# Performance work log

Hardware: AMD Instinct MI355X
Metric: run time of the kernel (lower is better)

The kernel has to match this reference:

```python
import jax, jax.numpy as jnp
import numpy as np

EPS_LN = 1e-6   # ln_1 / ln_2 (partial(LayerNorm, eps=1e-6))
EPS_ON = 1e-5   # SS2D out_norm (default LayerNorm eps)


def _ln(x, g, b, eps):
    m = jnp.mean(x, -1, keepdims=True)
    v = jnp.mean(jnp.square(x - m), -1, keepdims=True)
    return (x - m) * jax.lax.rsqrt(v + eps) * g + b


def _dwconv(x, w, b):
    # x: (B,C,H,W), w: (C,1,3,3) depthwise, 'SAME' padding (padding=1 for k=3)
    y = jax.lax.conv_general_dilated(x, w, (1, 1), 'SAME',
        feature_group_count=x.shape[1], dimension_numbers=('NCHW', 'OIHW', 'NCHW'))
    return y + b[None, :, None, None]


def _selective_scan(u, dts, A, Bs, Cs, Ds):
    # u, dts: (B,K,D,L); A: (K,D,N); Bs, Cs: (B,K,N,L); Ds: (K,D)
    B, K, D, L = u.shape
    N = A.shape[-1]
    uT = jnp.moveaxis(u, -1, 0)    # (L,B,K,D)
    dtT = jnp.moveaxis(dts, -1, 0)  # (L,B,K,D)
    BT = jnp.moveaxis(Bs, -1, 0)   # (L,B,K,N)
    CT = jnp.moveaxis(Cs, -1, 0)   # (L,B,K,N)

    def step(h, inp):
        u_t, dt_t, B_t, C_t = inp
        dA = jnp.exp(dt_t[..., None] * A)                                   # (B,K,D,N)
        h = dA * h + (dt_t * u_t)[..., None] * B_t[:, :, None, :]           # (B,K,D,N)
        y = jnp.einsum('bkdn,bkn->bkd', h, C_t)
        return h, y

    h0 = jnp.zeros((B, K, D, N), u.dtype)
    _, ys = jax.lax.scan(step, h0, (uT, dtT, BT, CT))
    ys = jnp.moveaxis(ys, 0, -1)   # (B,K,D,L)
    return ys + u * Ds[None, :, :, None]


def _ss2d(x, in_proj_w, conv_w, conv_b, x_proj_w, dt_w, dt_b, A_logs, Ds,
          onorm_g, onorm_b, out_proj_w):
    # x: (B,H,W,C) -> (B,H,W,C)
    B, H, W, C = x.shape
    Di = in_proj_w.shape[0] // 2
    K = x_proj_w.shape[0]
    R = dt_w.shape[-1]
    N = (x_proj_w.shape[1] - R) // 2
    L = H * W

    xz = x @ in_proj_w.T                       # (B,H,W,2*Di), bias=False
    xx, z = jnp.split(xz, 2, axis=-1)
    xx = jnp.transpose(xx, (0, 3, 1, 2))       # (B,Di,H,W)
    xx = jax.nn.silu(_dwconv(xx, conv_w, conv_b))

    # cross-scan: row-major, col-major, and their reversals
    x0 = xx.reshape(B, Di, L)
    x1 = jnp.transpose(xx, (0, 1, 3, 2)).reshape(B, Di, L)
    xs = jnp.stack([x0, x1, x0[..., ::-1], x1[..., ::-1]], axis=1)  # (B,K,Di,L)

    x_dbl = jnp.einsum('bkdl,kcd->bkcl', xs, x_proj_w)
    dts, Bs, Cs = jnp.split(x_dbl, [R, R + N], axis=2)
    dts = jnp.einsum('bkrl,kdr->bkdl', dts, dt_w)
    dts = jax.nn.softplus(dts + dt_b[None, :, :, None])
    A = -jnp.exp(A_logs.reshape(K, Di, N))

    ys = _selective_scan(xs, dts, A, Bs, Cs, Ds.reshape(K, Di))  # (B,K,Di,L)

    # cross-merge back to row-major
    y0 = ys[:, 0]
    y1 = jnp.transpose(ys[:, 1].reshape(B, Di, W, H), (0, 1, 3, 2)).reshape(B, Di, L)
    y2 = ys[:, 2, :, ::-1]
    y3 = jnp.transpose(ys[:, 3, :, ::-1].reshape(B, Di, W, H), (0, 1, 3, 2)).reshape(B, Di, L)
    y = jnp.transpose(y0 + y1 + y2 + y3, (0, 2, 1))              # (B,L,Di)
    y = _ln(y, onorm_g, onorm_b, EPS_ON).reshape(B, H, W, Di)
    y = y * jax.nn.silu(z)
    return y @ out_proj_w.T                    # bias=False


def setup_inputs() -> dict:
    key = jax.random.key(0)
    ks = jax.random.split(key, 16)
    B, H, W, C = 2, 56, 56, 192
    Di, N, K = 2 * C, 16, 4
    R = int(np.ceil(C / 16))                   # dt_rank = 12
    hid = 4 * C
    g = lambda k, shp, s=0.02: (jax.random.normal(k, shp) * s).astype(jnp.float32)
    return dict(
        x=jax.random.normal(ks[0], (B, H, W, C), jnp.float32),
        cpe1_w=g(ks[1], (C, 1, 3, 3), 0.1), cpe1_b=jnp.zeros((C,), jnp.float32),
        ln1_g=jnp.ones((C,), jnp.float32), ln1_b=jnp.zeros((C,), jnp.float32),
        in_proj_w=g(ks[2], (2 * Di, C)),
        conv_w=g(ks[3], (Di, 1, 3, 3), 0.1), conv_b=jnp.zeros((Di,), jnp.float32),
        x_proj_w=g(ks[4], (K, R + 2 * N, Di)),
        dt_w=g(ks[5], (K, Di, R), 0.1),
        dt_b=jnp.full((K, Di), float(np.log(np.expm1(0.01))), jnp.float32),
        A_logs=jnp.log(jnp.tile(jnp.arange(1, N + 1, dtype=jnp.float32), (K * Di, 1))),
        Ds=jnp.ones((K * Di,), jnp.float32),
        onorm_g=jnp.ones((Di,), jnp.float32), onorm_b=jnp.zeros((Di,), jnp.float32),
        out_proj_w=g(ks[6], (C, Di)),
        cpe2_w=g(ks[7], (C, 1, 3, 3), 0.1), cpe2_b=jnp.zeros((C,), jnp.float32),
        ln2_g=jnp.ones((C,), jnp.float32), ln2_b=jnp.zeros((C,), jnp.float32),
        fc1_w=g(ks[8], (hid, C)), fc1_b=jnp.zeros((hid,), jnp.float32),
        fc2_w=g(ks[9], (C, hid)), fc2_b=jnp.zeros((C,), jnp.float32),
    )


def reference(x, cpe1_w, cpe1_b, ln1_g, ln1_b, in_proj_w, conv_w, conv_b,
              x_proj_w, dt_w, dt_b, A_logs, Ds, onorm_g, onorm_b, out_proj_w,
              cpe2_w, cpe2_b, ln2_g, ln2_b, fc1_w, fc1_b, fc2_w, fc2_b):
    # x: (B,H,W,C)
    x = x + jnp.transpose(_dwconv(jnp.transpose(x, (0, 3, 1, 2)), cpe1_w, cpe1_b), (0, 2, 3, 1))
    x = x + _ss2d(_ln(x, ln1_g, ln1_b, EPS_LN), in_proj_w, conv_w, conv_b,
                  x_proj_w, dt_w, dt_b, A_logs, Ds, onorm_g, onorm_b, out_proj_w)
    x = x + jnp.transpose(_dwconv(jnp.transpose(x, (0, 3, 1, 2)), cpe2_w, cpe2_b), (0, 2, 3, 1))
    h = _ln(x, ln2_g, ln2_b, EPS_LN)
    h = jax.nn.gelu(h @ fc1_w.T + fc1_b, approximate=False)
    x = x + (h @ fc2_w.T + fc2_b)
    return x
```

## Files before the change

kernel.cpp:

```cpp
#include <hip/hip_runtime.h>
#include <math.h>

#define BB 2
#define HHH 56
#define WWW 56
#define CC 192
#define LL 3136
#define DI 384
#define KK 4
#define NN 16
#define RR 12
#define CP 44
#define HIDN 768
#define BL (BB*LL)
#define NCH 98
#define CHL 32

typedef __attribute__((ext_vector_type(8))) short bf16x8;
typedef __attribute__((ext_vector_type(4))) float f32x4;

__device__ __forceinline__ float siluf_(float x){ return x/(1.f+__expf(-x)); }
__device__ __forceinline__ float geluf_(float x){ return 0.5f*x*(1.f+erff(x*0.70710678118654752f)); }
__device__ __forceinline__ unsigned short bf16r_(float x){
  unsigned int u = __float_as_uint(x);
  u += 0x7FFFu + ((u>>16)&1u);
  return (unsigned short)(u>>16);
}
__device__ __forceinline__ float bf2f_(unsigned short u){
  return __uint_as_float(((unsigned int)u)<<16);
}

__global__ void k_cvtw(const float* __restrict__ s0, const float* __restrict__ s1,
                       const float* __restrict__ s2, const float* __restrict__ s3,
                       unsigned short* __restrict__ dst){
  int i = blockIdx.x*256 + threadIdx.x;
  if      (i < 147456) dst[i] = bf16r_(s0[i]);
  else if (i < 221184) dst[i] = bf16r_(s1[i-147456]);
  else if (i < 368640) dst[i] = bf16r_(s2[i-221184]);
  else if (i < 516096) dst[i] = bf16r_(s3[i-368640]);
}

__global__ void k_prepx(const float* __restrict__ xp, unsigned short* __restrict__ wXhi,
                        unsigned short* __restrict__ wXlo){
  int idx = blockIdx.x*256 + threadIdx.x;
  if (idx >= 192*384) return;
  int row = idx / 384, d = idx % 384;
  int k = row / 48, j = row % 48;
  float v = 0.f;
  if (j < 12) v = xp[(k*CP + j)*DI + d];
  else if (j >= 16) v = xp[(k*CP + (j-4))*DI + d];
  unsigned short hi = bf16r_(v);
  wXhi[idx] = hi;
  wXlo[idx] = bf16r_(v - bf2f_(hi));
}

__global__ void k_dwconv_res(const float* __restrict__ in, const float* __restrict__ wgt,
                             const float* __restrict__ bias, float* __restrict__ out) {
  int idx = blockIdx.x*256 + threadIdx.x;
  const int total = BB*HHH*WWW*CC;
  if (idx >= total) return;
  int c = idx % CC;
  int w = (idx / CC) % WWW;
  int h = (idx / (CC*WWW)) % HHH;
  int b = idx / (CC*WWW*HHH);
  float acc = bias[c];
  #pragma unroll
  for (int kh=0; kh<3; kh++){
    int hh = h + kh - 1; if (hh < 0 || hh >= HHH) continue;
    #pragma unroll
    for (int kw=0; kw<3; kw++){
      int ww = w + kw - 1; if (ww < 0 || ww >= WWW) continue;
      acc += in[((b*HHH+hh)*WWW+ww)*CC + c] * wgt[c*9 + kh*3 + kw];
    }
  }
  out[idx] = in[idx] + acc;
}

__global__ void k_ln192(const float* __restrict__ in, const float* __restrict__ g,
                        const float* __restrict__ bta, unsigned short* __restrict__ out, float eps) {
  int row = blockIdx.x*4 + (threadIdx.x>>6);
  int lane = threadIdx.x & 63;
  const float* p = in + (size_t)row*CC;
  float v0=p[lane], v1=p[lane+64], v2=p[lane+128];
  float s = v0+v1+v2, s2 = v0*v0+v1*v1+v2*v2;
  #pragma unroll
  for (int off=1; off<64; off<<=1){ s += __shfl_xor(s,off); s2 += __shfl_xor(s2,off); }
  float m = s*(1.f/192.f);
  float var = s2*(1.f/192.f) - m*m;
  float rstd = rsqrtf(var + eps);
  unsigned short* q = out + (size_t)row*CC;
  q[lane]     = bf16r_((v0-m)*rstd*g[lane]     + bta[lane]);
  q[lane+64]  = bf16r_((v1-m)*rstd*g[lane+64]  + bta[lane+64]);
  q[lane+128] = bf16r_((v2-m)*rstd*g[lane+128] + bta[lane+128]);
}

enum { EPI_NONE=0, EPI_RES=1, EPI_BIAS_GELU=2, EPI_BIAS_RES=3 };

template<int EPI, int OUTBF>
__global__ __launch_bounds__(256) void k_gemm_mfma(const unsigned short* __restrict__ A,
      const unsigned short* __restrict__ W, const float* __restrict__ bias,
      const float* __restrict__ res, void* __restrict__ outp, int M, int Nn, int Kk) {
  __shared__ unsigned short As[128][40];
  __shared__ unsigned short Bs[64][40];
  int tid = threadIdx.x;
  int m0 = blockIdx.y*128, n0 = blockIdx.x*64;
  int wid = tid>>6, lane = tid&63;
  int wm = wid*32;
  int fr = lane&15, fk = (lane>>4)*8;
  f32x4 acc[2][4];
  #pragma unroll
  for (int i=0;i<2;i++)
    #pragma unroll
    for (int j=0;j<4;j++) acc[i][j] = (f32x4){0.f,0.f,0.f,0.f};
  int arow = tid>>1, ak = (tid&1)*16;
  int wrow = tid>>2, wk = (tid&3)*8;
  const unsigned short* Ap = A + (size_t)(m0+arow)*Kk + ak;
  const unsigned short* Wp = W + (size_t)(n0+wrow)*Kk + wk;
  for (int k0=0; k0<Kk; k0+=32){
    __syncthreads();
    uint4 av0 = *(const uint4*)(Ap + k0);
    uint4 av1 = *(const uint4*)(Ap + k0 + 8);
    uint4 wv  = *(const uint4*)(Wp + k0);
    *(uint4*)&As[arow][ak]   = av0;
    *(uint4*)&As[arow][ak+8] = av1;
    *(uint4*)&Bs[wrow][wk]   = wv;
    __syncthreads();
    bf16x8 af[2], bfr[4];
    #pragma unroll
    for (int mi=0;mi<2;mi++) af[mi] = *(const bf16x8*)&As[wm + mi*16 + fr][fk];
    #pragma unroll
    for (int ni=0;ni<4;ni++) bfr[ni] = *(const bf16x8*)&Bs[ni*16 + fr][fk];
    #pragma unroll
    for (int mi=0;mi<2;mi++)
      #pragma unroll
      for (int ni=0;ni<4;ni++)
        acc[mi][ni] = __builtin_amdgcn_mfma_f32_16x16x32_bf16(af[mi], bfr[ni], acc[mi][ni], 0,0,0);
  }
  int rbase = (lane>>4)*4;
  #pragma unroll
  for (int mi=0;mi<2;mi++){
    #pragma unroll
    for (int ni=0;ni<4;ni++){
      int col = n0 + ni*16 + fr;
      float bv = (EPI==EPI_BIAS_GELU || EPI==EPI_BIAS_RES) ? bias[col] : 0.f;
      #pragma unroll
      for (int r=0;r<4;r++){
        int row = m0 + wm + mi*16 + rbase + r;
        float v = acc[mi][ni][r] + bv;
        if (EPI==EPI_BIAS_GELU) v = geluf_(v);
        if (EPI==EPI_RES || EPI==EPI_BIAS_RES) v += res[(size_t)row*Nn + col];
        if (OUTBF) ((unsigned short*)outp)[(size_t)row*Nn + col] = bf16r_(v);
        else       ((float*)outp)[(size_t)row*Nn + col] = v;
      }
    }
  }
}

__global__ __launch_bounds__(256) void k_xgemm(const float* __restrict__ uf,
      const unsigned short* __restrict__ wXhi, const unsigned short* __restrict__ wXlo,
      float* __restrict__ xdblT) {
  __shared__ unsigned short Ah[64][40];
  __shared__ unsigned short Al[64][40];
  __shared__ unsigned short Bh[64][40];
  __shared__ unsigned short Bl[64][40];
  int tid = threadIdx.x;
  int m0 = blockIdx.y*64, n0 = blockIdx.x*64;
  int wid = tid>>6, lane = tid&63;
  int fr = lane&15, fk = (lane>>4)*8;
  f32x4 acc[4];
  #pragma unroll
  for (int j=0;j<4;j++) acc[j] = (f32x4){0.f,0.f,0.f,0.f};
  int srow = tid>>2, sk = (tid&3)*8;
  const float* Ap = uf + (size_t)(m0+srow)*DI + sk;
  const unsigned short* Wh = wXhi + (size_t)(n0+srow)*DI + sk;
  const unsigned short* Wl = wXlo + (size_t)(n0+srow)*DI + sk;
  for (int k0=0; k0<DI; k0+=32){
    __syncthreads();
    float4 ua = *(const float4*)(Ap + k0);
    float4 ub = *(const float4*)(Ap + k0 + 4);
    uint4 wh = *(const uint4*)(Wh + k0);
    uint4 wl = *(const uint4*)(Wl + k0);
    float uv[8] = {ua.x,ua.y,ua.z,ua.w, ub.x,ub.y,ub.z,ub.w};
    #pragma unroll
    for (int j=0;j<8;j++){
      unsigned short hi = bf16r_(uv[j]);
      Ah[srow][sk+j] = hi;
      Al[srow][sk+j] = bf16r_(uv[j] - bf2f_(hi));
    }
    *(uint4*)&Bh[srow][sk] = wh;
    *(uint4*)&Bl[srow][sk] = wl;
    __syncthreads();
    bf16x8 ah = *(const bf16x8*)&Ah[wid*16 + fr][fk];
    bf16x8 al = *(const bf16x8*)&Al[wid*16 + fr][fk];
    #pragma unroll
    for (int ni=0;ni<4;ni++){
      bf16x8 bh = *(const bf16x8*)&Bh[ni*16 + fr][fk];
      bf16x8 bl = *(const bf16x8*)&Bl[ni*16 + fr][fk];
      acc[ni] = __builtin_amdgcn_mfma_f32_16x16x32_bf16(ah, bh, acc[ni], 0,0,0);
      acc[ni] = __builtin_amdgcn_mfma_f32_16x16x32_bf16(al, bh, acc[ni], 0,0,0);
      acc[ni] = __builtin_amdgcn_mfma_f32_16x16x32_bf16(ah, bl, acc[ni], 0,0,0);
    }
  }
  int rbase = (lane>>4)*4;
  #pragma unroll
  for (int ni=0;ni<4;ni++){
    int col = n0 + ni*16 + fr;
    int k = col / 48, j = col % 48;
    #pragma unroll
    for (int r=0;r<4;r++){
      int row = m0 + wid*16 + rbase + r;
      int b = row / LL, s = row % LL;
      int h = s / WWW, w2 = s % WWW;
      int l1 = w2*HHH + h;
      int lk = (k==0) ? s : (k==1) ? l1 : (k==2) ? (LL-1-s) : (LL-1-l1);
      xdblT[((size_t)((b*KK+k)*LL + lk))*48 + j] = acc[ni][r];
    }
  }
}

__global__ void k_conv_xx(const float* __restrict__ xz, const float* __restrict__ cw,
                          const float* __restrict__ cb, float* __restrict__ xc0,
                          float* __restrict__ xc1) {
  int idx = blockIdx.x*256 + threadIdx.x;
  if (idx >= BB*LL*DI) return;
  int d = idx % DI;
  int l = (idx / DI) % LL;
  int b = idx / (DI*LL);
  int h = l / WWW, w = l % WWW;
  float acc = cb[d];
  #pragma unroll
  for (int kh=0; kh<3; kh++){
    int hh = h + kh - 1; if (hh < 0 || hh >= HHH) continue;
    #pragma unroll
    for (int kw=0; kw<3; kw++){
      int ww2 = w + kw - 1; if (ww2 < 0 || ww2 >= WWW) continue;
      acc += xz[((size_t)(b*LL + hh*WWW + ww2))*(2*DI) + d] * cw[d*9 + kh*3 + kw];
    }
  }
  float v = siluf_(acc);
  xc0[idx] = v;
  xc1[((size_t)(b*LL + w*HHH + h))*DI + d] = v;
}

template<int PASS>
__global__ __launch_bounds__(64) void k_scan(const float* __restrict__ xc_l0,
        const float* __restrict__ xc_l1,
        const float* __restrict__ xdblT, const float* __restrict__ dtw, const float* __restrict__ dtb,
        const float* __restrict__ alogs, const float* __restrict__ Dsv,
        float* __restrict__ hend, float* __restrict__ sumdt, unsigned short* __restrict__ ysb) {
  int ch = blockIdx.y, bk = blockIdx.z;
  int b = bk >> 2, k = bk & 3;
  int d = blockIdx.x*64 + threadIdx.x;
  int kd = k*DI + d;
  float w[12];
  #pragma unroll
  for (int r=0;r<12;r++) w[r] = dtw[kd*12 + r];
  float biasd = dtb[kd];
  float Dd = (PASS==1) ? Dsv[kd] : 0.f;
  float An2[16];
  #pragma unroll
  for (int n=0;n<16;n++) An2[n] = -__expf(alogs[kd*16 + n]) * 1.44269504f;
  bool pw = true;
  #pragma unroll
  for (int n=1;n<16;n++) pw = pw && (fabsf(An2[n] - (float)(n+1)*An2[0]) <= 1e-3f*(float)(n+1)*fabsf(An2[0]));
  const float* usrc = (k & 1) ? xc_l1 : xc_l0;
  bool rev = (k >= 2);
  const float* rec0 = xdblT + ((size_t)bk*LL + ch*CHL)*48;
  float h[16];
  size_t hb = ((size_t)(bk*NCH + ch)*DI + d)*16;
  if (PASS==0){
    #pragma unroll
    for (int n=0;n<16;n++) h[n]=0.f;
  } else {
    #pragma unroll
    for (int n4=0;n4<4;n4++){
      float4 hv = *(const float4*)&hend[hb + n4*4];
      h[n4*4]=hv.x; h[n4*4+1]=hv.y; h[n4*4+2]=hv.z; h[n4*4+3]=hv.w;
    }
  }
  float cum = 0.f;
  #pragma unroll 2
  for (int i=0;i<CHL;i++){
    int li = ch*CHL + i;
    int lsrc = rev ? (LL-1-li) : li;
    float uu = usrc[((size_t)(b*LL + lsrc))*DI + d];
    const float* rec = rec0 + (size_t)i*48;
    float4 t0 = *(const float4*)(rec);
    float4 t1 = *(const float4*)(rec+4);
    float4 t2 = *(const float4*)(rec+8);
    float4 B0 = *(const float4*)(rec+16);
    float4 B1 = *(const float4*)(rec+20);
    float4 B2 = *(const float4*)(rec+24);
    float4 B3 = *(const float4*)(rec+28);
    float a0 = fmaf(t0.x,w[0], fmaf(t0.y,w[1], fmaf(t0.z,w[2], t0.w*w[3])));
    float a1 = fmaf(t1.x,w[4], fmaf(t1.y,w[5], fmaf(t1.z,w[6], t1.w*w[7])));
    float a2 = fmaf(t2.x,w[8], fmaf(t2.y,w[9], fmaf(t2.z,w[10], t2.w*w[11])));
    float a = biasd + a0 + (a1 + a2);
    float dt = 0.69314718f * log2f(1.f + exp2f(a*1.44269504f));
    float dtu = dt*uu;
    if (PASS==0) cum += dt;
    float dA[16];
    if (pw){
      float r = exp2f(dt*An2[0]);
      float p = r; dA[0] = p;
      #pragma unroll
      for (int n=1;n<16;n++){ p *= r; dA[n] = p; }
    } else {
      #pragma unroll
      for (int n=0;n<16;n++) dA[n] = exp2f(dt*An2[n]);
    }
    float Bv[16] = {B0.x,B0.y,B0.z,B0.w, B1.x,B1.y,B1.z,B1.w,
                    B2.x,B2.y,B2.z,B2.w, B3.x,B3.y,B3.z,B3.w};
    #pragma unroll
    for (int n=0;n<16;n++) h[n] = fmaf(dA[n], h[n], dtu*Bv[n]);
    if (PASS==1){
      float4 C0 = *(const float4*)(rec+32);
      float4 C1 = *(const float4*)(rec+36);
      float4 C2 = *(const float4*)(rec+40);
      float4 C3 = *(const float4*)(rec+44);
      float y0 = fmaf(h[0], C0.x, fmaf(h[1], C0.y, fmaf(h[2], C0.z, h[3]*C0.w)));
      float y1 = fmaf(h[4], C1.x, fmaf(h[5], C1.y, fmaf(h[6], C1.z, h[7]*C1.w)));
      float y2 = fmaf(h[8], C2.x, fmaf(h[9], C2.y, fmaf(h[10],C2.z, h[11]*C2.w)));
      float y3 = fmaf(h[12],C3.x, fmaf(h[13],C3.y, fmaf(h[14],C3.z, h[15]*C3.w)));
      float y = fmaf(uu, Dd, (y0+y1)+(y2+y3));
      ysb[((size_t)(bk*LL + li))*DI + d] = bf16r_(y);
    }
  }
  if (PASS==0){
    #pragma unroll
    for (int n4=0;n4<4;n4++)
      *(float4*)&hend[hb + n4*4] = make_float4(h[n4*4],h[n4*4+1],h[n4*4+2],h[n4*4+3]);
    sumdt[(bk*NCH + ch)*DI + d] = cum;
  }
}

__global__ __launch_bounds__(64) void k_scanmid(const float* __restrict__ alogs,
        const float* __restrict__ sumdt, float* __restrict__ hend) {
  int bid = blockIdx.x;
  int dblk = bid % 96;
  int k = (bid/96) % KK;
  int b = bid/(96*KK);
  int lane = threadIdx.x;
  int d4 = lane>>4, n = lane&15;
  int d = dblk*4 + d4;
  int bk = b*KK + k;
  float Ac2 = -__expf(alogs[(k*DI+d)*16 + n]) * 1.44269504f;
  float H = 0.f;
  for (int c=0;c<NCH;c++){
    float sdt = sumdt[(bk*NCH + c)*DI + d];
    float aexp = exp2f(Ac2 * sdt);
    size_t idx = ((size_t)(bk*NCH + c)*DI + dblk*4)*16 + lane;
    float tmp = hend[idx];
    hend[idx] = H;
    H = fmaf(aexp, H, tmp);
  }
}

__global__ __launch_bounds__(384) void k_fuse(const unsigned short* __restrict__ ysb,
      const float* __restrict__ xz, const float* __restrict__ og, const float* __restrict__ ob,
      unsigned short* __restrict__ a2) {
  __shared__ float sa[6], sb[6];
  int b = blockIdx.x / LL, l = blockIdx.x % LL;
  int d = threadIdx.x;
  int h_ = l / WWW, w_ = l % WWW;
  int l1 = w_*HHH + h_;
  float y = bf2f_(ysb[((size_t)((b*KK+0)*LL + l))*DI + d])
          + bf2f_(ysb[((size_t)((b*KK+1)*LL + l1))*DI + d])
          + bf2f_(ysb[((size_t)((b*KK+2)*LL + (LL-1-l)))*DI + d])
          + bf2f_(ysb[((size_t)((b*KK+3)*LL + (LL-1-l1)))*DI + d]);
  float s = y, s2 = y*y;
  #pragma unroll
  for (int off=1; off<64; off<<=1){ s += __shfl_xor(s,off); s2 += __shfl_xor(s2,off); }
  int wid = d >> 6;
  if ((d & 63) == 0){ sa[wid] = s; sb[wid] = s2; }
  __syncthreads();
  s = sa[0]+sa[1]+sa[2]+sa[3]+sa[4]+sa[5];
  s2 = sb[0]+sb[1]+sb[2]+sb[3]+sb[4]+sb[5];
  float m = s*(1.f/DI);
  float var = s2*(1.f/DI) - m*m;
  float rstd = rsqrtf(var + 1e-5f);
  float v = (y - m)*rstd*og[d] + ob[d];
  float z = xz[((size_t)(b*LL + l))*(2*DI) + DI + d];
  a2[((size_t)(b*LL + l))*DI + d] = bf16r_(v * siluf_(z));
}

extern "C" void kernel_launch(void* const* d_in, const int* in_sizes, int n_in,
                              void* d_out, int out_size, void* d_ws, size_t ws_size,
                              hipStream_t stream) {
  (void)in_sizes; (void)n_in; (void)out_size; (void)ws_size;
  const float* x       = (const float*)d_in[0];
  const float* cpe1_w  = (const float*)d_in[1];
  const float* cpe1_b  = (const float*)d_in[2];
  const float* ln1_g   = (const float*)d_in[3];
  const float* ln1_b   = (const float*)d_in[4];
  const float* in_proj = (const float*)d_in[5];
  const float* conv_w  = (const float*)d_in[6];
  const float* conv_b  = (const float*)d_in[7];
  const float* x_proj  = (const float*)d_in[8];
  const float* dt_w    = (const float*)d_in[9];
  const float* dt_b    = (const float*)d_in[10];
  const float* A_logs  = (const float*)d_in[11];
  const float* Dsv     = (const float*)d_in[12];
  const float* onorm_g = (const float*)d_in[13];
  const float* onorm_b = (const float*)d_in[14];
  const float* out_proj= (const float*)d_in[15];
  const float* cpe2_w  = (const float*)d_in[16];
  const float* cpe2_b  = (const float*)d_in[17];
  const float* ln2_g   = (const float*)d_in[18];
  const float* ln2_b   = (const float*)d_in[19];
  const float* fc1_w   = (const float*)d_in[20];
  const float* fc1_b   = (const float*)d_in[21];
  const float* fc2_w   = (const float*)d_in[22];
  const float* fc2_b   = (const float*)d_in[23];
  float* out = (float*)d_out;
  float* wsf = (float*)d_ws;

  float* x1    = wsf;
  float* xlnf  = x1 + 1204224;
  float* xz    = xlnf + 1204224;
  float* xc_l0 = xz + 4816896;
  float* xc_l1 = xc_l0 + 2408448;
  float* ysbf  = xc_l1 + 2408448;
  float* hend  = ysbf + 4816896;
  float* sumdt = hend + 4816896;
  float* xdblT = sumdt + 301056;
  unsigned short* wbf = (unsigned short*)(xdblT + 1204224);
  unsigned short* wXhi = (unsigned short*)(wbf + 516096);
  unsigned short* wXlo = wXhi + 73728;
  unsigned short* xln  = (unsigned short*)xlnf;
  unsigned short* xln2 = (unsigned short*)xlnf;
  unsigned short* ysb = (unsigned short*)ysbf;
  unsigned short* a2 = (unsigned short*)xdblT;
  float* x2   = xc_l0;
  float* x3   = xz;
  unsigned short* hbuf = (unsigned short*)ysbf;
  unsigned short* wIn  = wbf;
  unsigned short* wOut = wbf + 147456;
  unsigned short* wF1  = wbf + 221184;
  unsigned short* wF2  = wbf + 368640;

  k_cvtw<<<2016, 256, 0, stream>>>(in_proj, out_proj, fc1_w, fc2_w, wbf);
  k_prepx<<<288, 256, 0, stream>>>(x_proj, wXhi, wXlo);
  k_dwconv_res<<<(BB*HHH*WWW*CC+255)/256, 256, 0, stream>>>(x, cpe1_w, cpe1_b, x1);
  k_ln192<<<BL/4, 256, 0, stream>>>(x1, ln1_g, ln1_b, xln, 1e-6f);
  k_gemm_mfma<EPI_NONE,0><<<dim3(768/64, BL/128), 256, 0, stream>>>(xln, wIn, nullptr, nullptr, xz, BL, 2*DI, CC);
  k_conv_xx<<<(BB*LL*DI+255)/256, 256, 0, stream>>>(xz, conv_w, conv_b, xc_l0, xc_l1);
  k_xgemm<<<dim3(3, BL/64), 256, 0, stream>>>(xc_l0, wXhi, wXlo, xdblT);
  k_scan<0><<<dim3(6, NCH, BB*KK), 64, 0, stream>>>(xc_l0, xc_l1, xdblT, dt_w, dt_b, A_logs, Dsv, hend, sumdt, ysb);
  k_scanmid<<<BB*KK*96, 64, 0, stream>>>(A_logs, sumdt, hend);
  k_scan<1><<<dim3(6, NCH, BB*KK), 64, 0, stream>>>(xc_l0, xc_l1, xdblT, dt_w, dt_b, A_logs, Dsv, hend, sumdt, ysb);
  k_fuse<<<BB*LL, 384, 0, stream>>>(ysb, xz, onorm_g, onorm_b, a2);
  k_gemm_mfma<EPI_RES,0><<<dim3(192/64, BL/128), 256, 0, stream>>>(a2, wOut, nullptr, x1, x2, BL, CC, DI);
  k_dwconv_res<<<(BB*HHH*WWW*CC+255)/256, 256, 0, stream>>>(x2, cpe2_w, cpe2_b, x3);
  k_ln192<<<BL/4, 256, 0, stream>>>(x3, ln2_g, ln2_b, xln2, 1e-6f);
  k_gemm_mfma<EPI_BIAS_GELU,1><<<dim3(768/64, BL/128), 256, 0, stream>>>(xln2, wF1, fc1_b, nullptr, hbuf, BL, HIDN, CC);
  k_gemm_mfma<EPI_BIAS_RES,0><<<dim3(192/64, BL/128), 256, 0, stream>>>(hbuf, wF2, fc2_b, x3, out, BL, CC, HIDN);
}
```

Before: 246.6 us.

## Store scan chunk states in bf16, use 64-row GEMM tiles for narrow outputs

The chunk-boundary SSM state buffer (hend) is now stored as bf16 instead of fp32, which halves its traffic across scan pass 0, the mid-pass combine and scan pass 1. The GEMM kernel gains an M-tile template parameter, and the two N=192 GEMMs (out_proj and fc2) switch to 64-row tiles so they launch more blocks. The power computation for dA uses a shallower multiplication tree instead of a serial chain of multiplies. Rounding the states to bf16 adds precision error to the scan carries.

```diff
diff --git a/kernel.cpp b/kernel.cpp
--- a/kernel.cpp
+++ b/kernel.cpp
@@ -96,52 +96,59 @@
 
 enum { EPI_NONE=0, EPI_RES=1, EPI_BIAS_GELU=2, EPI_BIAS_RES=3 };
 
-template<int EPI, int OUTBF>
+template<int MT, int EPI, int OUTBF>
 __global__ __launch_bounds__(256) void k_gemm_mfma(const unsigned short* __restrict__ A,
       const unsigned short* __restrict__ W, const float* __restrict__ bias,
       const float* __restrict__ res, void* __restrict__ outp, int M, int Nn, int Kk) {
-  __shared__ unsigned short As[128][40];
+  __shared__ unsigned short As[MT][40];
   __shared__ unsigned short Bs[64][40];
+  constexpr int NI = (MT==128) ? 4 : 2;
   int tid = threadIdx.x;
-  int m0 = blockIdx.y*128, n0 = blockIdx.x*64;
+  int m0 = blockIdx.y*MT, n0 = blockIdx.x*64;
   int wid = tid>>6, lane = tid&63;
-  int wm = wid*32;
+  int wm = (MT==128) ? wid*32 : (wid&1)*32;
+  int wn = (MT==128) ? 0 : (wid>>1)*32;
   int fr = lane&15, fk = (lane>>4)*8;
-  f32x4 acc[2][4];
+  f32x4 acc[2][NI];
   #pragma unroll
   for (int i=0;i<2;i++)
     #pragma unroll
-    for (int j=0;j<4;j++) acc[i][j] = (f32x4){0.f,0.f,0.f,0.f};
-  int arow = tid>>1, ak = (tid&1)*16;
+    for (int j=0;j<NI;j++) acc[i][j] = (f32x4){0.f,0.f,0.f,0.f};
+  int arow, ak;
+  if (MT==128){ arow = tid>>1; ak = (tid&1)*16; }
+  else        { arow = tid>>2; ak = (tid&3)*8;  }
   int wrow = tid>>2, wk = (tid&3)*8;
   const unsigned short* Ap = A + (size_t)(m0+arow)*Kk + ak;
   const unsigned short* Wp = W + (size_t)(n0+wrow)*Kk + wk;
   for (int k0=0; k0<Kk; k0+=32){
     __syncthreads();
-    uint4 av0 = *(const uint4*)(Ap + k0);
-    uint4 av1 = *(const uint4*)(Ap + k0 + 8);
-    uint4 wv  = *(const uint4*)(Wp + k0);
-    *(uint4*)&As[arow][ak]   = av0;
-    *(uint4*)&As[arow][ak+8] = av1;
-    *(uint4*)&Bs[wrow][wk]   = wv;
+    if (MT==128){
+      uint4 av0 = *(const uint4*)(Ap + k0);
+      uint4 av1 = *(const uint4*)(Ap + k0 + 8);
+      *(uint4*)&As[arow][ak]   = av0;
+      *(uint4*)&As[arow][ak+8] = av1;
+    } else {
+      *(uint4*)&As[arow][ak] = *(const uint4*)(Ap + k0);
+    }
+    *(uint4*)&Bs[wrow][wk] = *(const uint4*)(Wp + k0);
     __syncthreads();
-    bf16x8 af[2], bfr[4];
+    bf16x8 af[2], bfr[NI];
     #pragma unroll
     for (int mi=0;mi<2;mi++) af[mi] = *(const bf16x8*)&As[wm + mi*16 + fr][fk];
     #pragma unroll
-    for (int ni=0;ni<4;ni++) bfr[ni] = *(const bf16x8*)&Bs[ni*16 + fr][fk];
+    for (int ni=0;ni<NI;ni++) bfr[ni] = *(const bf16x8*)&Bs[wn + ni*16 + fr][fk];
     #pragma unroll
     for (int mi=0;mi<2;mi++)
       #pragma unroll
-      for (int ni=0;ni<4;ni++)
+      for (int ni=0;ni<NI;ni++)
         acc[mi][ni] = __builtin_amdgcn_mfma_f32_16x16x32_bf16(af[mi], bfr[ni], acc[mi][ni], 0,0,0);
   }
   int rbase = (lane>>4)*4;
   #pragma unroll
   for (int mi=0;mi<2;mi++){
     #pragma unroll
-    for (int ni=0;ni<4;ni++){
-      int col = n0 + ni*16 + fr;
+    for (int ni=0;ni<NI;ni++){
+      int col = n0 + wn + ni*16 + fr;
       float bv = (EPI==EPI_BIAS_GELU || EPI==EPI_BIAS_RES) ? bias[col] : 0.f;
       #pragma unroll
       for (int r=0;r<4;r++){
@@ -247,7 +254,7 @@
         const float* __restrict__ xc_l1,
         const float* __restrict__ xdblT, const float* __restrict__ dtw, const float* __restrict__ dtb,
         const float* __restrict__ alogs, const float* __restrict__ Dsv,
-        float* __restrict__ hend, float* __restrict__ sumdt, unsigned short* __restrict__ ysb) {
+        unsigned short* __restrict__ hend, float* __restrict__ sumdt, unsigned short* __restrict__ ysb) {
   int ch = blockIdx.y, bk = blockIdx.z;
   int b = bk >> 2, k = bk & 3;
   int d = blockIdx.x*64 + threadIdx.x;
@@ -272,10 +279,13 @@
     #pragma unroll
     for (int n=0;n<16;n++) h[n]=0.f;
   } else {
-    #pragma unroll
-    for (int n4=0;n4<4;n4++){
-      float4 hv = *(const float4*)&hend[hb + n4*4];
-      h[n4*4]=hv.x; h[n4*4+1]=hv.y; h[n4*4+2]=hv.z; h[n4*4+3]=hv.w;
+    uint4 q0 = *(const uint4*)&hend[hb];
+    uint4 q1 = *(const uint4*)&hend[hb+8];
+    unsigned int qa[8] = {q0.x,q0.y,q0.z,q0.w, q1.x,q1.y,q1.z,q1.w};
+    #pragma unroll
+    for (int j=0;j<8;j++){
+      h[2*j]   = bf2f_((unsigned short)(qa[j] & 0xffffu));
+      h[2*j+1] = bf2f_((unsigned short)(qa[j] >> 16));
     }
   }
   float cum = 0.f;
@@ -301,10 +311,15 @@
     if (PASS==0) cum += dt;
     float dA[16];
     if (pw){
-      float r = exp2f(dt*An2[0]);
-      float p = r; dA[0] = p;
-      #pragma unroll
-      for (int n=1;n<16;n++){ p *= r; dA[n] = p; }
+      float r1 = exp2f(dt*An2[0]);
+      float r2 = r1*r1;
+      float r3 = r2*r1;
+      float r4 = r2*r2;
+      float r8 = r4*r4;
+      dA[0]=r1;     dA[1]=r2;     dA[2]=r3;     dA[3]=r4;
+      dA[4]=r4*r1;  dA[5]=r4*r2;  dA[6]=r4*r3;  dA[7]=r8;
+      dA[8]=r8*r1;  dA[9]=r8*r2;  dA[10]=r8*r3; dA[11]=r8*r4;
+      dA[12]=r8*dA[4]; dA[13]=r8*dA[5]; dA[14]=r8*dA[6]; dA[15]=r8*r8;
     } else {
       #pragma unroll
       for (int n=0;n<16;n++) dA[n] = exp2f(dt*An2[n]);
@@ -327,15 +342,18 @@
     }
   }
   if (PASS==0){
-    #pragma unroll
-    for (int n4=0;n4<4;n4++)
-      *(float4*)&hend[hb + n4*4] = make_float4(h[n4*4],h[n4*4+1],h[n4*4+2],h[n4*4+3]);
+    unsigned int pk[8];
+    #pragma unroll
+    for (int j=0;j<8;j++)
+      pk[j] = ((unsigned int)bf16r_(h[2*j+1])<<16) | (unsigned int)bf16r_(h[2*j]);
+    *(uint4*)&hend[hb]   = make_uint4(pk[0],pk[1],pk[2],pk[3]);
+    *(uint4*)&hend[hb+8] = make_uint4(pk[4],pk[5],pk[6],pk[7]);
     sumdt[(bk*NCH + ch)*DI + d] = cum;
   }
 }
 
 __global__ __launch_bounds__(64) void k_scanmid(const float* __restrict__ alogs,
-        const float* __restrict__ sumdt, float* __restrict__ hend) {
+        const float* __restrict__ sumdt, unsigned short* __restrict__ hend) {
   int bid = blockIdx.x;
   int dblk = bid % 96;
   int k = (bid/96) % KK;
@@ -350,8 +368,8 @@
     float sdt = sumdt[(bk*NCH + c)*DI + d];
     float aexp = exp2f(Ac2 * sdt);
     size_t idx = ((size_t)(bk*NCH + c)*DI + dblk*4)*16 + lane;
-    float tmp = hend[idx];
-    hend[idx] = H;
+    float tmp = bf2f_(hend[idx]);
+    hend[idx] = bf16r_(H);
     H = fmaf(aexp, H, tmp);
   }
 }
@@ -421,16 +439,17 @@
   float* xc_l0 = xz + 4816896;
   float* xc_l1 = xc_l0 + 2408448;
   float* ysbf  = xc_l1 + 2408448;
-  float* hend  = ysbf + 4816896;
-  float* sumdt = hend + 4816896;
+  float* hendf = ysbf + 4816896;
+  float* sumdt = hendf + 2408448;
   float* xdblT = sumdt + 301056;
   unsigned short* wbf = (unsigned short*)(xdblT + 1204224);
-  unsigned short* wXhi = (unsigned short*)(wbf + 516096);
+  unsigned short* wXhi = wbf + 516096;
   unsigned short* wXlo = wXhi + 73728;
   unsigned short* xln  = (unsigned short*)xlnf;
   unsigned short* xln2 = (unsigned short*)xlnf;
-  unsigned short* ysb = (unsigned short*)ysbf;
-  unsigned short* a2 = (unsigned short*)xdblT;
+  unsigned short* ysb  = (unsigned short*)ysbf;
+  unsigned short* hend = (unsigned short*)hendf;
+  unsigned short* a2   = (unsigned short*)xdblT;
   float* x2   = xc_l0;
   float* x3   = xz;
   unsigned short* hbuf = (unsigned short*)ysbf;
@@ -443,16 +462,16 @@
   k_prepx<<<288, 256, 0, stream>>>(x_proj, wXhi, wXlo);
   k_dwconv_res<<<(BB*HHH*WWW*CC+255)/256, 256, 0, stream>>>(x, cpe1_w, cpe1_b, x1);
   k_ln192<<<BL/4, 256, 0, stream>>>(x1, ln1_g, ln1_b, xln, 1e-6f);
-  k_gemm_mfma<EPI_NONE,0><<<dim3(768/64, BL/128), 256, 0, stream>>>(xln, wIn, nullptr, nullptr, xz, BL, 2*DI, CC);
+  k_gemm_mfma<128,EPI_NONE,0><<<dim3(768/64, BL/128), 256, 0, stream>>>(xln, wIn, nullptr, nullptr, xz, BL, 2*DI, CC);
   k_conv_xx<<<(BB*LL*DI+255)/256, 256, 0, stream>>>(xz, conv_w, conv_b, xc_l0, xc_l1);
   k_xgemm<<<dim3(3, BL/64), 256, 0, stream>>>(xc_l0, wXhi, wXlo, xdblT);
   k_scan<0><<<dim3(6, NCH, BB*KK), 64, 0, stream>>>(xc_l0, xc_l1, xdblT, dt_w, dt_b, A_logs, Dsv, hend, sumdt, ysb);
   k_scanmid<<<BB*KK*96, 64, 0, stream>>>(A_logs, sumdt, hend);
   k_scan<1><<<dim3(6, NCH, BB*KK), 64, 0, stream>>>(xc_l0, xc_l1, xdblT, dt_w, dt_b, A_logs, Dsv, hend, sumdt, ysb);
   k_fuse<<<BB*LL, 384, 0, stream>>>(ysb, xz, onorm_g, onorm_b, a2);
-  k_gemm_mfma<EPI_RES,0><<<dim3(192/64, BL/128), 256, 0, stream>>>(a2, wOut, nullptr, x1, x2, BL, CC, DI);
+  k_gemm_mfma<64,EPI_RES,0><<<dim3(192/64, BL/64), 256, 0, stream>>>(a2, wOut, nullptr, x1, x2, BL, CC, DI);
   k_dwconv_res<<<(BB*HHH*WWW*CC+255)/256, 256, 0, stream>>>(x2, cpe2_w, cpe2_b, x3);
   k_ln192<<<BL/4, 256, 0, stream>>>(x3, ln2_g, ln2_b, xln2, 1e-6f);
-  k_gemm_mfma<EPI_BIAS_GELU,1><<<dim3(768/64, BL/128), 256, 0, stream>>>(xln2, wF1, fc1_b, nullptr, hbuf, BL, HIDN, CC);
-  k_gemm_mfma<EPI_BIAS_RES,0><<<dim3(192/64, BL/128), 256, 0, stream>>>(hbuf, wF2, fc2_b, x3, out, BL, CC, HIDN);
-}
+  k_gemm_mfma<128,EPI_BIAS_GELU,1><<<dim3(768/64, BL/128), 256, 0, stream>>>(xln2, wF1, fc1_b, nullptr, hbuf, BL, HIDN, CC);
+  k_gemm_mfma<64,EPI_BIAS_RES,0><<<dim3(192/64, BL/64), 256, 0, stream>>>(hbuf, wF2, fc2_b, x3, out, BL, CC, HIDN);
+}
```

Measured after the change: 243.0 us. About the same (-1.5%).
